# Performance work log

Measured on AMD Instinct MI355X. Metric: run time of the kernel, lower is better.

Reference implementation:

```python
import jax, jax.numpy as jnp
import numpy as np

N_NODES = 50000


def gcn_conv(x, edge_index, W, b, num_nodes):
    """PyG GCNConv: add self-loops, symmetric norm, gather-scatter aggregate."""
    h = x @ W  # [N, out]
    row = jnp.concatenate([edge_index[0], jnp.arange(num_nodes)])  # sources (+ self loops)
    col = jnp.concatenate([edge_index[1], jnp.arange(num_nodes)])  # targets
    deg = jax.ops.segment_sum(jnp.ones_like(col, dtype=h.dtype), col, num_segments=num_nodes)
    dinv = jnp.where(deg > 0, jax.lax.rsqrt(deg), 0.0)
    norm = dinv[row] * dinv[col]  # [E+N]
    msgs = h[row] * norm[:, None]  # gather + scale
    out = jax.ops.segment_sum(msgs, col, num_segments=num_nodes)  # scatter-add
    return out + b


def setup_inputs() -> dict:
    key = jax.random.key(0)
    ks = jax.random.split(key, 8)
    F_in, H, D = 50, 50, 64
    E_train, Ep, En = 1600000, 200000, 200000
    x = jax.random.normal(ks[0], (N_NODES, F_in), dtype=jnp.float32)
    train_pos_edge_index = jax.random.randint(ks[1], (2, E_train), 0, N_NODES)
    pos_edge_index = jax.random.randint(ks[2], (2, Ep), 0, N_NODES)
    neg_edge_index = jax.random.randint(ks[3], (2, En), 0, N_NODES)
    # Glorot-ish params for the two GCN layers
    W1 = jax.random.normal(ks[4], (F_in, H), dtype=jnp.float32) * (1.0 / np.sqrt(F_in))
    b1 = jnp.zeros((H,), dtype=jnp.float32)
    W2 = jax.random.normal(ks[5], (H, D), dtype=jnp.float32) * (1.0 / np.sqrt(H))
    b2 = jnp.zeros((D,), dtype=jnp.float32)
    return {"x": x, "train_pos_edge_index": train_pos_edge_index,
            "pos_edge_index": pos_edge_index, "neg_edge_index": neg_edge_index,
            "W1": W1, "b1": b1, "W2": W2, "b2": b2}


def reference(x, train_pos_edge_index, pos_edge_index, neg_edge_index, W1, b1, W2, b2):
    # encode: conv1 -> relu -> conv2
    h = gcn_conv(x, train_pos_edge_index, W1, b1, N_NODES)
    h = jax.nn.relu(h)
    z = gcn_conv(h, train_pos_edge_index, W2, b2, N_NODES)  # [N, D]
    # decode: dot product over concatenated pos/neg edge endpoints
    edge_index = jnp.concatenate([pos_edge_index, neg_edge_index], axis=-1)
    logits = jnp.sum(z[edge_index[0]] * z[edge_index[1]], axis=-1)  # [Ep+En]
    return logits
```

## Files before the change

kernel.cpp:

```cpp
#include <hip/hip_runtime.h>
#include <hip/hip_bf16.h>
#include <hip/hip_fp16.h>


constexpr int N_NODES = 50000;
constexpr int NBITS = 6;
constexpr int BNODES = 1 << NBITS;
constexpr int NBUCK = (N_NODES + BNODES - 1) / BNODES;
constexpr int CAP = 2560;
constexpr int CHUNK = 6144;
constexpr int PTHREADS = 1024;
constexpr int CTHREADS = 512;
constexpr int NTILE = 8;
constexpr int TROWS = 6250;
constexpr int H1STRIDE = 7;

union H4 {
    uint2 u;
    __half2 h[2];
};

union H8 {
    uint4 u;
    __half2 h[4];
};

__device__ inline H4 f4_to_h4(float4 v) {
    H4 r;
    r.h[0] = __floats2half2_rn(v.x, v.y);
    r.h[1] = __floats2half2_rn(v.z, v.w);
    return r;
}

__device__ inline uint4 pack8(float4 A, float4 B) {
    H8 r;
    r.h[0] = __floats2half2_rn(A.x, A.y);
    r.h[1] = __floats2half2_rn(A.z, A.w);
    r.h[2] = __floats2half2_rn(B.x, B.y);
    r.h[3] = __floats2half2_rn(B.z, B.w);
    return r.u;
}

__device__ inline void unpack8(uint4 w, int* r) {
    r[0] = (int)(w.x & 0xffffu);  r[1] = (int)(w.x >> 16);
    r[2] = (int)(w.y & 0xffffu);  r[3] = (int)(w.y >> 16);
    r[4] = (int)(w.z & 0xffffu);  r[5] = (int)(w.z >> 16);
    r[6] = (int)(w.w & 0xffffu);  r[7] = (int)(w.w >> 16);
}

__device__ inline void add8(float4& A, float4& B, H8 v) {
    float2 g0 = __half22float2(v.h[0]);
    float2 g1 = __half22float2(v.h[1]);
    float2 g2 = __half22float2(v.h[2]);
    float2 g3 = __half22float2(v.h[3]);
    A.x += g0.x; A.y += g0.y; A.z += g1.x; A.w += g1.y;
    B.x += g2.x; B.y += g2.y; B.z += g3.x; B.w += g3.y;
}

__device__ inline void fma8(float4& A, float4& B, H8 v, float m) {
    float2 g0 = __half22float2(v.h[0]);
    float2 g1 = __half22float2(v.h[1]);
    float2 g2 = __half22float2(v.h[2]);
    float2 g3 = __half22float2(v.h[3]);
    A.x = fmaf(m, g0.x, A.x); A.y = fmaf(m, g0.y, A.y);
    A.z = fmaf(m, g1.x, A.z); A.w = fmaf(m, g1.y, A.w);
    B.x = fmaf(m, g2.x, B.x); B.y = fmaf(m, g2.y, B.y);
    B.z = fmaf(m, g3.x, B.z); B.w = fmaf(m, g3.y, B.w);
}

__device__ inline float hdot2(unsigned ua, unsigned ub) {
    __half2 ha = *(__half2*)&ua;
    __half2 hb = *(__half2*)&ub;
    float2 fa = __half22float2(ha);
    float2 fb = __half22float2(hb);
    return fa.x * fb.x + fa.y * fb.y;
}

__global__ __launch_bounds__(PTHREADS) void partition_kernel(const int4* __restrict__ row4,
                                                             const int4* __restrict__ col4, int E,
                                                             int* __restrict__ cursor,
                                                             unsigned* __restrict__ bEdges) {
    __shared__ unsigned ed2[CHUNK];
    __shared__ unsigned char tick[CHUNK];
    __shared__ int cnt[NBUCK];
    __shared__ int loff[NBUCK];
    __shared__ int base[NBUCK];
    int t = threadIdx.x;
    int e0 = blockIdx.x * CHUNK;
    int n = min(CHUNK, E - e0);
    int n4 = n >> 2;
    for (int i = t; i < NBUCK; i += PTHREADS) cnt[i] = 0;
    __syncthreads();
    const int4* r4 = row4 + (e0 >> 2);
    const int4* c4 = col4 + (e0 >> 2);
    for (int i = t; i < n4; i += PTHREADS) {
        int4 c = c4[i];
        tick[i * 4 + 0] = (unsigned char)atomicAdd(&cnt[c.x >> NBITS], 1);
        tick[i * 4 + 1] = (unsigned char)atomicAdd(&cnt[c.y >> NBITS], 1);
        tick[i * 4 + 2] = (unsigned char)atomicAdd(&cnt[c.z >> NBITS], 1);
        tick[i * 4 + 3] = (unsigned char)atomicAdd(&cnt[c.w >> NBITS], 1);
    }
    __syncthreads();
    if (t < 64) {
        constexpr int SEG = (NBUCK + 63) / 64;
        int lo = t * SEG;
        int hi = min(lo + SEG, NBUCK);
        int s = 0;
        for (int i = lo; i < hi; ++i) {
            loff[i] = s;
            s += cnt[i];
        }
        int tot = s;
        int ex = tot;
#pragma unroll
        for (int off = 1; off < 64; off <<= 1) {
            int o = __shfl_up(ex, off, 64);
            if (t >= off) ex += o;
        }
        ex -= tot;
        for (int i = lo; i < hi; ++i) loff[i] += ex;
    }
    __syncthreads();
    for (int i = t; i < NBUCK; i += PTHREADS) base[i] = cnt[i] ? atomicAdd(&cursor[i], cnt[i]) : 0;
    for (int i = t; i < n4; i += PTHREADS) {
        int4 r = r4[i];
        int4 c = c4[i];
        unsigned p0 = ((unsigned)r.x << 16) | (unsigned)c.x;
        unsigned p1 = ((unsigned)r.y << 16) | (unsigned)c.y;
        unsigned p2 = ((unsigned)r.z << 16) | (unsigned)c.z;
        unsigned p3 = ((unsigned)r.w << 16) | (unsigned)c.w;
        ed2[loff[c.x >> NBITS] + (int)tick[i * 4 + 0]] = p0;
        ed2[loff[c.y >> NBITS] + (int)tick[i * 4 + 1]] = p1;
        ed2[loff[c.z >> NBITS] + (int)tick[i * 4 + 2]] = p2;
        ed2[loff[c.w >> NBITS] + (int)tick[i * 4 + 3]] = p3;
    }
    __syncthreads();
    for (int s = t; s < n; s += PTHREADS) {
        unsigned p = ed2[s];
        int bk = (int)(p & 0xffffu) >> NBITS;
        int pos = base[bk] + (s - loff[bk]);
        if (pos < CAP) bEdges[(size_t)bk * CAP + pos] = p;
    }
}

__global__ __launch_bounds__(CTHREADS) void bucket_csr_mm_kernel(const int* __restrict__ cursor,
                                                                 const unsigned* __restrict__ bEdges,
                                                                 const float* __restrict__ x,
                                                                 const float* __restrict__ W1,
                                                                 unsigned short* __restrict__ srcIdx,
                                                                 unsigned* __restrict__ rowmeta,
                                                                 float* __restrict__ dinv,
                                                                 uint2* __restrict__ Hs, int N) {
    __shared__ alignas(16) unsigned short srcL[CAP];
    __shared__ unsigned char tick[CAP];
    __shared__ int tdeg[BNODES * NTILE];
    __shared__ int toff[BNODES * NTILE];
    __shared__ int totPad;
    __shared__ float dinvL[BNODES];
    __shared__ float4 Ws4[50 * 16];
    int b = blockIdx.x;
    int tx = threadIdx.x;
    int cnt = min(cursor[b], CAP);
    for (int i = tx; i < BNODES * NTILE; i += CTHREADS) tdeg[i] = 0;
    {
        uint4* z4 = (uint4*)srcL;
        uint4 z = make_uint4(0u, 0u, 0u, 0u);
        for (int i = tx; i < (CAP >> 3); i += CTHREADS) z4[i] = z;
    }
    __syncthreads();
    const uint4* s4 = (const uint4*)(bEdges + (size_t)b * CAP);
    int cnt4 = cnt >> 2;
    for (int i = tx; i < cnt4; i += CTHREADS) {
        uint4 w = s4[i];
        unsigned pp[4] = {w.x, w.y, w.z, w.w};
#pragma unroll
        for (int u = 0; u < 4; ++u) {
            unsigned p = pp[u];
            int l = (int)(p & (BNODES - 1));
            int tl = (int)(p >> 16) / TROWS;
            tick[i * 4 + u] = (unsigned char)atomicAdd(&tdeg[l * NTILE + tl], 1);
        }
    }
    for (int i = cnt4 * 4 + tx; i < cnt; i += CTHREADS) {
        unsigned p = bEdges[(size_t)b * CAP + i];
        int l = (int)(p & (BNODES - 1));
        int tl = (int)(p >> 16) / TROWS;
        tick[i] = (unsigned char)atomicAdd(&tdeg[l * NTILE + tl], 1);
    }
    for (int i = tx; i < 50 * 64; i += CTHREADS) {
        int k = i >> 6;
        int c = i & 63;
        ((float*)Ws4)[i] = (c < 50) ? W1[k * 50 + c] : 0.f;
    }
    __syncthreads();
    if (tx < BNODES) {
        int sd[NTILE];
        int d = 0;
#pragma unroll
        for (int u = 0; u < NTILE; ++u) {
            sd[u] = tdeg[tx * NTILE + u];
            d += sd[u];
        }
        int dpad = (d + 7) & ~7;
        int s = dpad;
#pragma unroll
        for (int off = 1; off < BNODES; off <<= 1) {
            int o = __shfl_up(s, off, 64);
            if (tx >= off) s += o;
        }
        int ex = s - dpad;
        int run = ex;
#pragma unroll
        for (int u = 0; u < NTILE; ++u) {
            toff[tx * NTILE + u] = run;
            run += sd[u];
        }
        if (tx == 63) totPad = min(s, CAP);
        float dvv = rsqrtf((float)d + 1.0f);
        dinvL[tx] = dvv;
        int node = b * BNODES + tx;
        if (node < N) {
            unsigned st = (unsigned)(b * CAP + ex);
            rowmeta[node] = (st << 7) | (unsigned)d;
            dinv[node] = dvv;
        }
    }
    __syncthreads();
    for (int i = tx; i < cnt4; i += CTHREADS) {
        uint4 w = s4[i];
        unsigned pp[4] = {w.x, w.y, w.z, w.w};
#pragma unroll
        for (int u = 0; u < 4; ++u) {
            unsigned p = pp[u];
            int l = (int)(p & (BNODES - 1));
            int tl = (int)(p >> 16) / TROWS;
            int pos = toff[l * NTILE + tl] + (int)tick[i * 4 + u];
            if (pos < CAP) srcL[pos] = (unsigned short)(p >> 16);
        }
    }
    for (int i = cnt4 * 4 + tx; i < cnt; i += CTHREADS) {
        unsigned p = bEdges[(size_t)b * CAP + i];
        int l = (int)(p & (BNODES - 1));
        int tl = (int)(p >> 16) / TROWS;
        int pos = toff[l * NTILE + tl] + (int)tick[i];
        if (pos < CAP) srcL[pos] = (unsigned short)(p >> 16);
    }
    __syncthreads();
    int tot = totPad;
    {
        const uint4* sl4 = (const uint4*)srcL;
        uint4* si4 = (uint4*)(srcIdx + (size_t)b * CAP);
        for (int i = tx; i < (tot >> 3); i += CTHREADS) si4[i] = sl4[i];
    }
    int q = tx & 15;
    int g = tx >> 4;
#pragma unroll
    for (int rep = 0; rep < 2; ++rep) {
        int l = g + rep * 32;
        int node = b * BNODES + l;
        const float* xr = x + (size_t)min(node, N - 1) * 50;
        float4 acc = make_float4(0.f, 0.f, 0.f, 0.f);
#pragma unroll
        for (int k = 0; k < 50; ++k) {
            float xv = xr[k];
            float4 w = Ws4[k * 16 + q];
            acc.x = fmaf(xv, w.x, acc.x);
            acc.y = fmaf(xv, w.y, acc.y);
            acc.z = fmaf(xv, w.z, acc.z);
            acc.w = fmaf(xv, w.w, acc.w);
        }
        float dv = dinvL[l];
        acc.x *= dv;
        acc.y *= dv;
        acc.z *= dv;
        acc.w *= dv;
        if (node < N && q < 2 * H1STRIDE) Hs[(size_t)node * (2 * H1STRIDE) + q] = f4_to_h4(acc).u;
    }
}

template <int STRIDE>
__device__ inline void gather_sum8(const unsigned short* __restrict__ srcIdx,
                                   const uint4* __restrict__ hs, int node, int q,
                                   unsigned meta, float4& A, float4& B) {
    int start = (int)(meta >> 7);
    int d = (int)(meta & 127u);
    int end = start + d;
    H8 t;
    t.u = hs[(size_t)node * STRIDE + q];
    {
        float2 g0 = __half22float2(t.h[0]);
        float2 g1 = __half22float2(t.h[1]);
        float2 g2 = __half22float2(t.h[2]);
        float2 g3 = __half22float2(t.h[3]);
        A = make_float4(g0.x, g0.y, g1.x, g1.y);
        B = make_float4(g2.x, g2.y, g3.x, g3.y);
    }
    if (d == 0) return;
    int j = start;
    uint4 w = *(const uint4*)(srcIdx + j);
    while (j + 8 <= end) {
        uint4 wc = w;
        if (j + 8 < end) w = *(const uint4*)(srcIdx + j + 8);
        int r[8];
        unpack8(wc, r);
#pragma unroll
        for (int u = 0; u < 8; ++u) {
            H8 hv;
            hv.u = hs[(size_t)r[u] * STRIDE + q];
            add8(A, B, hv);
        }
        j += 8;
    }
    if (j < end) {
        int r[8];
        unpack8(w, r);
#pragma unroll
        for (int u = 0; u < 8; ++u) {
            float m = (j + u < end) ? 1.f : 0.f;
            H8 hv;
            hv.u = hs[(size_t)r[u] * STRIDE + q];
            fma8(A, B, hv, m);
        }
    }
}

template <int BC>
__global__ __launch_bounds__(256) void agg_mm_kernel(const unsigned* __restrict__ rowmeta,
                                                     const unsigned short* __restrict__ srcIdx,
                                                     const uint4* __restrict__ hs,
                                                     const float* __restrict__ dinv,
                                                     const float* __restrict__ b1,
                                                     const float* __restrict__ W2,
                                                     uint4* __restrict__ out, int N) {
    __shared__ float4 Ws4[50 * 16];
    __shared__ float h1s[32][68];
    for (int i = threadIdx.x; i < 50 * 64; i += 256) ((float*)Ws4)[i] = W2[i];
    int tid = blockIdx.x * blockDim.x + threadIdx.x;
    int node = tid >> 3;
    int q = tid & 7;
    int g = threadIdx.x >> 3;
    int nodeC = min(node, N - 1);
    float4 A = make_float4(0.f, 0.f, 0.f, 0.f), B = A;
    if (q < 7) gather_sum8<H1STRIDE>(srcIdx, hs, nodeC, q, rowmeta[nodeC], A, B);
    float dv = dinv[nodeC];
    int f = q * 8;
    float hv[8] = {A.x, A.y, A.z, A.w, B.x, B.y, B.z, B.w};
#pragma unroll
    for (int u = 0; u < 8; ++u) {
        float bb = (f + u < BC) ? b1[f + u] : 0.f;
        h1s[g][f + u] = fmaxf(dv * hv[u] + bb, 0.f);
    }
    __syncthreads();
    float4 aA = make_float4(0.f, 0.f, 0.f, 0.f), aB = aA;
#pragma unroll
    for (int k = 0; k < 50; ++k) {
        float xv = h1s[g][k];
        float4 wA = Ws4[k * 16 + 2 * q];
        float4 wB = Ws4[k * 16 + 2 * q + 1];
        aA.x = fmaf(xv, wA.x, aA.x);
        aA.y = fmaf(xv, wA.y, aA.y);
        aA.z = fmaf(xv, wA.z, aA.z);
        aA.w = fmaf(xv, wA.w, aA.w);
        aB.x = fmaf(xv, wB.x, aB.x);
        aB.y = fmaf(xv, wB.y, aB.y);
        aB.z = fmaf(xv, wB.z, aB.z);
        aB.w = fmaf(xv, wB.w, aB.w);
    }
    aA.x *= dv; aA.y *= dv; aA.z *= dv; aA.w *= dv;
    aB.x *= dv; aB.y *= dv; aB.z *= dv; aB.w *= dv;
    if (node < N) out[(size_t)node * 8 + q] = pack8(aA, aB);
}

template <int BC>
__global__ __launch_bounds__(256) void agg_kernel(const unsigned* __restrict__ rowmeta,
                                                  const unsigned short* __restrict__ srcIdx,
                                                  const uint4* __restrict__ hs,
                                                  const float* __restrict__ dinv,
                                                  const float* __restrict__ b,
                                                  uint4* __restrict__ out, int N) {
    int tid = blockIdx.x * blockDim.x + threadIdx.x;
    int node = tid >> 3;
    int q = tid & 7;
    if (node >= N) return;
    float4 A, B;
    gather_sum8<8>(srcIdx, hs, node, q, rowmeta[node], A, B);
    float dv = dinv[node];
    int f = q * 8;
    float hv[8] = {A.x, A.y, A.z, A.w, B.x, B.y, B.z, B.w};
    float o[8];
#pragma unroll
    for (int u = 0; u < 8; ++u) o[u] = dv * hv[u] + (f + u < BC ? b[f + u] : 0.f);
    out[(size_t)node * 8 + q] =
        pack8(make_float4(o[0], o[1], o[2], o[3]), make_float4(o[4], o[5], o[6], o[7]));
}

__global__ __launch_bounds__(256) void decode_kernel(const int* __restrict__ pos,
                                                     const int* __restrict__ neg, int Ep, int En,
                                                     const uint4* __restrict__ z4,
                                                     float* __restrict__ logits) {
    int tid = blockIdx.x * blockDim.x + threadIdx.x;
    int e = tid >> 3;
    int q = tid & 7;
    int Etot = Ep + En;
    if (e >= Etot) return;
    int a, bn;
    if (e < Ep) {
        a = pos[e];
        bn = pos[Ep + e];
    } else {
        int t = e - Ep;
        a = neg[t];
        bn = neg[En + t];
    }
    uint4 ua = z4[(size_t)a * 8 + q];
    uint4 ub = z4[(size_t)bn * 8 + q];
    float v = hdot2(ua.x, ub.x) + hdot2(ua.y, ub.y) + hdot2(ua.z, ub.z) + hdot2(ua.w, ub.w);
    v += __shfl_xor(v, 1, 64);
    v += __shfl_xor(v, 2, 64);
    v += __shfl_xor(v, 4, 64);
    if (q == 0) logits[e] = v;
}

extern "C" void kernel_launch(void* const* d_in, const int* in_sizes, int n_in,
                              void* d_out, int out_size, void* d_ws, size_t ws_size,
                              hipStream_t stream) {
    const float* x = (const float*)d_in[0];
    const int* train = (const int*)d_in[1];
    const int* pos = (const int*)d_in[2];
    const int* neg = (const int*)d_in[3];
    const float* W1 = (const float*)d_in[4];
    const float* b1 = (const float*)d_in[5];
    const float* W2 = (const float*)d_in[6];
    const float* b2 = (const float*)d_in[7];
    float* logits = (float*)d_out;

    const int FIN = 50;
    const int N = in_sizes[0] / FIN;
    const int E = in_sizes[1] / 2;
    const int Ep = in_sizes[2] / 2;
    const int En = in_sizes[3] / 2;

    const int* t_row = train;
    const int* t_col = train + E;

    float* dinv = (float*)d_ws;
    __half* buf0 = (__half*)(dinv + N);
    __half* buf1 = buf0 + (size_t)N * 64;
    unsigned* rowmeta = (unsigned*)(buf1 + (size_t)N * 64);
    int* cursor = (int*)(rowmeta + N);
    uintptr_t sp = (uintptr_t)(cursor + NBUCK);
    sp = (sp + 15) & ~(uintptr_t)15;
    unsigned short* srcIdx = (unsigned short*)sp;
    uintptr_t bp = (uintptr_t)(srcIdx + (size_t)NBUCK * CAP);
    bp = (bp + 15) & ~(uintptr_t)15;
    unsigned* bEdges = (unsigned*)bp;

    (void)hipMemsetAsync(cursor, 0, (size_t)NBUCK * sizeof(int), stream);

    partition_kernel<<<(E + CHUNK - 1) / CHUNK, PTHREADS, 0, stream>>>((const int4*)t_row,
                                                                       (const int4*)t_col, E,
                                                                       cursor, bEdges);
    bucket_csr_mm_kernel<<<NBUCK, CTHREADS, 0, stream>>>(cursor, bEdges, x, W1, srcIdx, rowmeta,
                                                         dinv, (uint2*)buf0, N);

    const int AGB = (N * 8 + 255) / 256;

    agg_mm_kernel<50><<<AGB, 256, 0, stream>>>(rowmeta, srcIdx, (const uint4*)buf0, dinv, b1, W2,
                                               (uint4*)buf1, N);
    agg_kernel<64><<<AGB, 256, 0, stream>>>(rowmeta, srcIdx, (const uint4*)buf1, dinv, b2,
                                            (uint4*)buf0, N);
    decode_kernel<<<((Ep + En) * 8 + 255) / 256, 256, 0, stream>>>(pos, neg, Ep, En,
                                                                   (const uint4*)buf0, logits);
}
```

Before: 183.3 us.

## Fuse aggregation, second layer and decode into one cooperative persistent kernel

Replaces the three tail kernels (layer-1 aggregate with the W2 matmul, layer-2 aggregate, edge decode) with one cooperative kernel of 1024 persistent blocks that separates the stages with grid.sync. It is meant to remove kernel launch overhead and the gaps between launches. If the cooperative launch fails, the code falls back to the original three launches. In exchange, each stage loops over virtual blocks, occupancy is capped by the launch bounds, and grid-wide barriers add their own cost.

```diff
diff --git a/kernel.cpp b/kernel.cpp
--- a/kernel.cpp
+++ b/kernel.cpp
@@ -1,6 +1,9 @@
 #include <hip/hip_runtime.h>
 #include <hip/hip_bf16.h>
 #include <hip/hip_fp16.h>
+#include <hip/hip_cooperative_groups.h>
+
+namespace cg = cooperative_groups;
 
 
 constexpr int N_NODES = 50000;
@@ -14,6 +17,7 @@
 constexpr int NTILE = 8;
 constexpr int TROWS = 6250;
 constexpr int H1STRIDE = 7;
+constexpr int COOPB = 1024;
 
 union H4 {
     uint2 u;
@@ -280,7 +284,7 @@
 
 template <int STRIDE>
 __device__ inline void gather_sum8(const unsigned short* __restrict__ srcIdx,
-                                   const uint4* __restrict__ hs, int node, int q,
+                                   const uint4* hs, int node, int q,
                                    unsigned meta, float4& A, float4& B) {
     int start = (int)(meta >> 7);
     int d = (int)(meta & 127u);
@@ -321,6 +325,98 @@
             hv.u = hs[(size_t)r[u] * STRIDE + q];
             fma8(A, B, hv, m);
         }
+    }
+}
+
+__global__ __launch_bounds__(256, 4) void fused_tail_kernel(
+    const unsigned* __restrict__ rowmeta, const unsigned short* __restrict__ srcIdx,
+    const uint4* hs1, const float* __restrict__ dinv, const float* __restrict__ b1,
+    const float* __restrict__ W2, uint4* __restrict__ hs2, uint4* z,
+    const int* __restrict__ pos, const int* __restrict__ neg,
+    const float* __restrict__ b2v, float* __restrict__ logits,
+    int Ep, int En, int N) {
+    cg::grid_group grid = cg::this_grid();
+    __shared__ float4 Ws4[50 * 16];
+    __shared__ float h1s[32][68];
+    for (int i = threadIdx.x; i < 50 * 64; i += 256) ((float*)Ws4)[i] = W2[i];
+    const int NB1 = (N * 8 + 255) / 256;
+    int g = threadIdx.x >> 3;
+    for (int vb = blockIdx.x; vb < NB1; vb += gridDim.x) {
+        int tid = vb * 256 + threadIdx.x;
+        int node = tid >> 3;
+        int q = tid & 7;
+        int nodeC = min(node, N - 1);
+        float4 A = make_float4(0.f, 0.f, 0.f, 0.f), B = A;
+        if (q < 7) gather_sum8<H1STRIDE>(srcIdx, hs1, nodeC, q, rowmeta[nodeC], A, B);
+        float dv = dinv[nodeC];
+        int f = q * 8;
+        float hv[8] = {A.x, A.y, A.z, A.w, B.x, B.y, B.z, B.w};
+#pragma unroll
+        for (int u = 0; u < 8; ++u) {
+            float bb = (f + u < 50) ? b1[f + u] : 0.f;
+            h1s[g][f + u] = fmaxf(dv * hv[u] + bb, 0.f);
+        }
+        __syncthreads();
+        float4 aA = make_float4(0.f, 0.f, 0.f, 0.f), aB = aA;
+#pragma unroll
+        for (int k = 0; k < 50; ++k) {
+            float xv = h1s[g][k];
+            float4 wA = Ws4[k * 16 + 2 * q];
+            float4 wB = Ws4[k * 16 + 2 * q + 1];
+            aA.x = fmaf(xv, wA.x, aA.x);
+            aA.y = fmaf(xv, wA.y, aA.y);
+            aA.z = fmaf(xv, wA.z, aA.z);
+            aA.w = fmaf(xv, wA.w, aA.w);
+            aB.x = fmaf(xv, wB.x, aB.x);
+            aB.y = fmaf(xv, wB.y, aB.y);
+            aB.z = fmaf(xv, wB.z, aB.z);
+            aB.w = fmaf(xv, wB.w, aB.w);
+        }
+        aA.x *= dv; aA.y *= dv; aA.z *= dv; aA.w *= dv;
+        aB.x *= dv; aB.y *= dv; aB.z *= dv; aB.w *= dv;
+        if (node < N) hs2[(size_t)node * 8 + q] = pack8(aA, aB);
+        __syncthreads();
+    }
+    grid.sync();
+    for (int vb = blockIdx.x; vb < NB1; vb += gridDim.x) {
+        int tid = vb * 256 + threadIdx.x;
+        int node = tid >> 3;
+        int q = tid & 7;
+        if (node < N) {
+            float4 A, B;
+            gather_sum8<8>(srcIdx, hs2, node, q, rowmeta[node], A, B);
+            float dv = dinv[node];
+            int f = q * 8;
+            float hv[8] = {A.x, A.y, A.z, A.w, B.x, B.y, B.z, B.w};
+            float o[8];
+#pragma unroll
+            for (int u = 0; u < 8; ++u) o[u] = dv * hv[u] + b2v[f + u];
+            z[(size_t)node * 8 + q] =
+                pack8(make_float4(o[0], o[1], o[2], o[3]), make_float4(o[4], o[5], o[6], o[7]));
+        }
+    }
+    grid.sync();
+    int Etot = Ep + En;
+    int total = Etot * 8;
+    for (int tid = blockIdx.x * 256 + threadIdx.x; tid < total; tid += gridDim.x * 256) {
+        int e = tid >> 3;
+        int q = tid & 7;
+        int a, bn;
+        if (e < Ep) {
+            a = pos[e];
+            bn = pos[Ep + e];
+        } else {
+            int t2 = e - Ep;
+            a = neg[t2];
+            bn = neg[En + t2];
+        }
+        uint4 ua = z[(size_t)a * 8 + q];
+        uint4 ub = z[(size_t)bn * 8 + q];
+        float v = hdot2(ua.x, ub.x) + hdot2(ua.y, ub.y) + hdot2(ua.z, ub.z) + hdot2(ua.w, ub.w);
+        v += __shfl_xor(v, 1, 64);
+        v += __shfl_xor(v, 2, 64);
+        v += __shfl_xor(v, 4, 64);
+        if (q == 0) logits[e] = v;
     }
 }
 
@@ -463,12 +559,30 @@
     bucket_csr_mm_kernel<<<NBUCK, CTHREADS, 0, stream>>>(cursor, bEdges, x, W1, srcIdx, rowmeta,
                                                          dinv, (uint2*)buf0, N);
 
-    const int AGB = (N * 8 + 255) / 256;
-
-    agg_mm_kernel<50><<<AGB, 256, 0, stream>>>(rowmeta, srcIdx, (const uint4*)buf0, dinv, b1, W2,
-                                               (uint4*)buf1, N);
-    agg_kernel<64><<<AGB, 256, 0, stream>>>(rowmeta, srcIdx, (const uint4*)buf1, dinv, b2,
-                                            (uint4*)buf0, N);
-    decode_kernel<<<((Ep + En) * 8 + 255) / 256, 256, 0, stream>>>(pos, neg, Ep, En,
-                                                                   (const uint4*)buf0, logits);
-}
+    const unsigned* rm = rowmeta;
+    const unsigned short* si = srcIdx;
+    const uint4* hs1c = (const uint4*)buf0;
+    const float* dvc = dinv;
+    const float* b1c = b1;
+    const float* W2c = W2;
+    uint4* hs2c = (uint4*)buf1;
+    uint4* zc = (uint4*)buf0;
+    const int* posc = pos;
+    const int* negc = neg;
+    const float* b2c = b2;
+    float* lgc = logits;
+    int Epv = Ep, Env = En, Nv = N;
+    void* args[] = {&rm, &si, &hs1c, &dvc, &b1c, &W2c, &hs2c, &zc,
+                    &posc, &negc, &b2c, &lgc, &Epv, &Env, &Nv};
+    hipError_t cerr = hipLaunchCooperativeKernel((const void*)fused_tail_kernel, dim3(COOPB),
+                                                 dim3(256), args, 0, stream);
+    if (cerr != hipSuccess) {
+        const int AGB = (N * 8 + 255) / 256;
+        agg_mm_kernel<50><<<AGB, 256, 0, stream>>>(rowmeta, srcIdx, (const uint4*)buf0, dinv, b1,
+                                                   W2, (uint4*)buf1, N);
+        agg_kernel<64><<<AGB, 256, 0, stream>>>(rowmeta, srcIdx, (const uint4*)buf1, dinv, b2,
+                                                (uint4*)buf0, N);
+        decode_kernel<<<((Ep + En) * 8 + 255) / 256, 256, 0, stream>>>(pos, neg, Ep, En,
+                                                                       (const uint4*)buf0, logits);
+    }
+}
```

After: 463.8 us. +153.0%, slower.
